# Performance work log

Measured on AMD Instinct MI355X. Metric: run time of the kernel, lower is better.

Reference implementation:

```python
import jax, jax.numpy as jnp
import numpy as np

SEQ_LEN = 2048
WIN = 2
LAYERS = 3
D_MODEL = 512
TDA_DIM = 7
TDA_WEIGHT = 0.3


def _nan0(x):
    return jnp.where(jnp.isnan(x), jnp.zeros_like(x), x)


def _tda_features(x):
    # x: [B, T, D] -> [B, 7]; vectorized version of the per-(b,d) stats loop
    B, T, D = x.shape
    mean = x.mean(axis=1)                                  # [B, D]
    std = x.std(axis=1, ddof=1)                            # torch.std is unbiased
    mn = x.min(axis=1)
    mx = x.max(axis=1)
    idx = jnp.arange(T, dtype=x.dtype)
    xc = x - mean[:, None, :]
    ic = idx - idx.mean()
    trend = _nan0(jnp.einsum('btd,t->bd', xc, ic) /
                  jnp.sqrt((xc * xc).sum(axis=1) * (ic * ic).sum()))
    # lag-1 autocorrelation via corrcoef of (x[:-1], x[1:])
    a = x[:, :-1, :]; b = x[:, 1:, :]
    ac = a - a.mean(axis=1, keepdims=True)
    bc = b - b.mean(axis=1, keepdims=True)
    autocorr = _nan0((ac * bc).sum(axis=1) /
                     jnp.sqrt((ac * ac).sum(axis=1) * (bc * bc).sum(axis=1)))
    # spectral centroid over first T//2 bins of |fft|^2 (== |rfft|^2 there)
    half = T // 2
    ps = jnp.abs(jnp.fft.rfft(x, axis=1)[:, :half, :]) ** 2  # [B, half, D]
    centroid = _nan0(jnp.einsum('btd,t->bd', ps, idx[:half]) / ps.sum(axis=1))
    feats = jnp.stack([mean, std, mn, mx, trend, autocorr, centroid], axis=-1)  # [B, D, 7]
    return feats.mean(axis=1)  # mean over channels -> [B, 7]


def _freq_interp(x, src_len, tgt_len):
    # x: [B, D, src_len] -> [B, D, tgt_len]; zero-pad/truncate in rfft domain
    xf = jnp.fft.rfft(x, axis=2)
    tgt_f = tgt_len // 2 + 1
    copy = min(xf.shape[2], tgt_f)
    out_f = jnp.zeros(x.shape[:2] + (tgt_f,), dtype=xf.dtype).at[:, :, :copy].set(xf[:, :, :copy])
    return jnp.fft.irfft(out_f, n=tgt_len, axis=2) * (src_len / tgt_len)


def _forward(levels, w1, b1, w2, b2, inj_w, inj_b):
    tda = _tda_features(levels[0])                              # [B, 7]
    h = jnp.maximum(tda @ w1 + b1, 0.0)
    attn = jax.nn.sigmoid(h @ w2 + b2)[:, None, :]              # [B, 1, D]
    rev = levels[::-1]
    n = len(rev)
    out_low, out_high = rev[0], rev[1]
    outs = [out_low]
    num_inj = LAYERS + 1
    for i in range(n - 1):
        src = SEQ_LEN // WIN ** (LAYERS - i)
        tgt = SEQ_LEN // WIN ** (LAYERS - i - 1)
        res = _freq_interp(out_low.transpose(0, 2, 1), src, tgt).transpose(0, 2, 1)
        left = (out_high - res) * attn
        safe_idx = (n - i - 2) % num_inj
        left = left + TDA_WEIGHT * (tda @ inj_w[safe_idx] + inj_b[safe_idx])[:, None, :]
        out_low = out_high
        if i + 2 <= n - 1:
            out_high = rev[i + 2]
        outs.append(left)
    return tuple(outs[::-1])


def setup_inputs() -> dict:
    key = jax.random.key(0)
    ks = jax.random.split(key, 20)
    B = 32
    inp = {}
    for l in range(LAYERS + 1):
        T = SEQ_LEN // WIN ** l
        inp[f'level{l}'] = jax.random.normal(ks[l], (B, T, D_MODEL), dtype=jnp.float32)
    s7 = 1.0 / np.sqrt(TDA_DIM)
    sd = 1.0 / np.sqrt(D_MODEL)
    inp['w1'] = jax.random.normal(ks[4], (TDA_DIM, D_MODEL), dtype=jnp.float32) * s7
    inp['b1'] = jnp.zeros((D_MODEL,), dtype=jnp.float32)
    inp['w2'] = jax.random.normal(ks[5], (D_MODEL, D_MODEL), dtype=jnp.float32) * sd
    inp['b2'] = jnp.zeros((D_MODEL,), dtype=jnp.float32)
    for j in range(LAYERS + 1):
        inp[f'wi{j}'] = jax.random.normal(ks[6 + j], (TDA_DIM, D_MODEL), dtype=jnp.float32) * s7
        inp[f'bi{j}'] = jnp.zeros((D_MODEL,), dtype=jnp.float32)
    return inp


def reference(level0, level1, level2, level3, w1, b1, w2, b2,
              wi0, bi0, wi1, bi1, wi2, bi2, wi3, bi3):
    levels = [level0, level1, level2, level3]
    inj_w = [wi0, wi1, wi2, wi3]
    inj_b = [bi0, bi1, bi2, bi3]
    return _forward(levels, w1, b1, w2, b2, inj_w, inj_b)
```

## Files before the change

kernel.cpp:

```cpp
#include <hip/hip_runtime.h>
#include <math.h>

constexpr int B  = 32;
constexpr int T0 = 2048;
constexpr int D  = 512;

constexpr size_t OFF_PART = 0;
constexpr size_t OFF_ATTN = OFF_PART + (size_t)B * 64 * 8;
constexpr size_t OFF_INJ  = OFF_ATTN + (size_t)B * D;

typedef float nfloat4 __attribute__((ext_vector_type(4)));

template<int LO>
__device__ __forceinline__ void wredt_add(float& v) {
  #pragma unroll
  for (int off = 32; off >= LO; off >>= 1) v += __shfl_down(v, off);
}
template<int LO>
__device__ __forceinline__ void wredt_min(float& v) {
  #pragma unroll
  for (int off = 32; off >= LO; off >>= 1) v = fminf(v, __shfl_down(v, off));
}
template<int LO>
__device__ __forceinline__ void wredt_max(float& v) {
  #pragma unroll
  for (int off = 32; off >= LO; off >>= 1) v = fmaxf(v, __shfl_down(v, off));
}
__device__ __forceinline__ void wred_add(float& v) { wredt_add<4>(v); }

__device__ __forceinline__ void nt_store4(float* p, float4 v) {
  nfloat4 nv;
  nv.x = v.x; nv.y = v.y; nv.z = v.z; nv.w = v.w;
  __builtin_nontemporal_store(nv, (nfloat4*)p);
}

__device__ __forceinline__ float4 cadd(float4 a, float4 b) {
  return make_float4(a.x+b.x, a.y+b.y, a.z+b.z, a.w+b.w);
}
__device__ __forceinline__ float4 csub(float4 a, float4 b) {
  return make_float4(a.x-b.x, a.y-b.y, a.z-b.z, a.w-b.w);
}
__device__ __forceinline__ float4 cmul(float4 v, float2 w) {
  return make_float4(v.x*w.x - v.y*w.y, v.x*w.y + v.y*w.x,
                     v.z*w.x - v.w*w.y, v.z*w.y + v.w*w.x);
}
__device__ __forceinline__ float4 cmulc(float4 v, float2 w) {
  return make_float4(v.x*w.x + v.y*w.y, v.y*w.x - v.x*w.y,
                     v.z*w.x + v.w*w.y, v.w*w.x - v.z*w.y);
}
__device__ __forceinline__ float4 cmul_mi(float4 v) {
  return make_float4(v.y, -v.x, v.w, -v.z);
}
__device__ __forceinline__ float4 cmul_pi(float4 v) {
  return make_float4(-v.y, v.x, -v.w, v.z);
}

__global__ __launch_bounds__(512) void k_tda(const float* __restrict__ x,
                                              float* __restrict__ part) {
  __shared__ float4 buf[T0 * 2];
  __shared__ float2 tw[1024];
  __shared__ float perd[8][8];
  float* scr = (float*)tw;
  const int tid  = threadIdx.x;
  const int L = blockIdx.x + 64 * blockIdx.y;
  const int m = (L >> 3) & 1;
  const int q = (L & 7) | ((L >> 4) << 3);
  const int eb = (q & 31) * 2 + m;
  const int b  = q >> 5;
  const int f    = tid & 1;
  const int rIdx = tid >> 1;
  const int lane = tid & 63;
  const int wv   = tid >> 6;
  const float* base = x + (size_t)b * T0 * D + eb * 8 + f * 4;

  float4 s1 = {0,0,0,0}, s2 = {0,0,0,0}, st = {0,0,0,0};
  float4 mn = {INFINITY,INFINITY,INFINITY,INFINITY};
  float4 mx = {-INFINITY,-INFINITY,-INFINITY,-INFINITY};
  #pragma unroll
  for (int u = 0; u < 8; ++u) {
    int t = rIdx + 256 * u;
    float4 v = *(const float4*)&base[(size_t)t * D];
    buf[t * 2 + f] = v;
    float tf = (float)t;
    s1.x += v.x; s1.y += v.y; s1.z += v.z; s1.w += v.w;
    s2.x = fmaf(v.x,v.x,s2.x); s2.y = fmaf(v.y,v.y,s2.y);
    s2.z = fmaf(v.z,v.z,s2.z); s2.w = fmaf(v.w,v.w,s2.w);
    st.x = fmaf(tf,v.x,st.x); st.y = fmaf(tf,v.y,st.y);
    st.z = fmaf(tf,v.z,st.z); st.w = fmaf(tf,v.w,st.w);
    mn.x = fminf(mn.x,v.x); mn.y = fminf(mn.y,v.y); mn.z = fminf(mn.z,v.z); mn.w = fminf(mn.w,v.w);
    mx.x = fmaxf(mx.x,v.x); mx.y = fmaxf(mx.y,v.y); mx.z = fmaxf(mx.z,v.z); mx.w = fmaxf(mx.w,v.w);
  }
  __syncthreads();
  float4 cc = {0,0,0,0};
  #pragma unroll
  for (int u = 0; u < 8; ++u) {
    int t = rIdx + 256 * u;
    if (t < T0 - 1) {
      float4 a = buf[t * 2 + f];
      float4 nb = buf[(t + 1) * 2 + f];
      cc.x = fmaf(a.x,nb.x,cc.x); cc.y = fmaf(a.y,nb.y,cc.y);
      cc.z = fmaf(a.z,nb.z,cc.z); cc.w = fmaf(a.w,nb.w,cc.w);
    }
  }
  wredt_add<2>(s1.x); wredt_add<2>(s1.y); wredt_add<2>(s1.z); wredt_add<2>(s1.w);
  wredt_add<2>(s2.x); wredt_add<2>(s2.y); wredt_add<2>(s2.z); wredt_add<2>(s2.w);
  wredt_add<2>(st.x); wredt_add<2>(st.y); wredt_add<2>(st.z); wredt_add<2>(st.w);
  wredt_add<2>(cc.x); wredt_add<2>(cc.y); wredt_add<2>(cc.z); wredt_add<2>(cc.w);
  wredt_min<2>(mn.x); wredt_min<2>(mn.y); wredt_min<2>(mn.z); wredt_min<2>(mn.w);
  wredt_max<2>(mx.x); wredt_max<2>(mx.y); wredt_max<2>(mx.z); wredt_max<2>(mx.w);
  if (lane < 2) {
    float* p = scr + ((size_t)wv * 2 + f) * 24;
    p[0]=s1.x; p[1]=s2.x; p[2]=st.x; p[3]=cc.x; p[4]=mn.x; p[5]=mx.x;
    p[6]=s1.y; p[7]=s2.y; p[8]=st.y; p[9]=cc.y; p[10]=mn.y; p[11]=mx.y;
    p[12]=s1.z; p[13]=s2.z; p[14]=st.z; p[15]=cc.z; p[16]=mn.z; p[17]=mx.z;
    p[18]=s1.w; p[19]=s2.w; p[20]=st.w; p[21]=cc.w; p[22]=mn.w; p[23]=mx.w;
  }
  __syncthreads();
  if (tid < 8) {
    const int dl = tid;
    const int fq = dl >> 2, c = dl & 3;
    float S1=0.f, S2=0.f, St=0.f, C=0.f, MN=INFINITY, MX=-INFINITY;
    for (int w = 0; w < 8; ++w) {
      const float* p = scr + ((size_t)w * 2 + fq) * 24 + c * 6;
      S1 += p[0]; S2 += p[1]; St += p[2]; C += p[3];
      MN = fminf(MN, p[4]); MX = fmaxf(MX, p[5]);
    }
    const float x0 = ((const float*)buf)[dl];
    const float xl = ((const float*)buf)[(size_t)(T0 - 1) * 8 + dl];
    const float Tf = (float)T0;
    const float mean = S1 / Tf;
    const float sxx  = S2 - S1 * S1 / Tf;
    const float stdv = sqrtf(fmaxf(sxx / (Tf - 1.f), 0.f));
    const float tbar = (Tf - 1.f) * 0.5f;
    const float Sic  = Tf * (Tf * Tf - 1.f) / 12.f;
    float trend = (St - tbar * S1) / sqrtf(sxx * Sic);
    if (isnan(trend)) trend = 0.f;
    const float na = Tf - 1.f;
    const float Sa = S1 - xl, Sb = S1 - x0;
    const float an  = C - Sa * Sb / na;
    const float sa2 = (S2 - xl * xl) - Sa * Sa / na;
    const float sb2 = (S2 - x0 * x0) - Sb * Sb / na;
    float ac = an / sqrtf(sa2 * sb2);
    if (isnan(ac)) ac = 0.f;
    perd[dl][0] = mean; perd[dl][1] = stdv; perd[dl][2] = MN;
    perd[dl][3] = MX;   perd[dl][4] = trend; perd[dl][5] = ac;
  }
  __syncthreads();

  for (int k = tid; k < 1024; k += 512) {
    float sw, cw;
    sincosf(-(float)M_PI * (float)k * (1.0f / 1024.0f), &sw, &cw);
    tw[k] = make_float2(cw, sw);
  }
  __syncthreads();

  for (int stg = 0; stg < 10; stg += 2) {
    const int lg = 10 - stg;
    const int h = 1 << lg;
    #pragma unroll
    for (int it = 0; it < 2; ++it) {
      int sl = it * 512 + tid;
      int pp = sl & 1;
      int qi = sl >> 1;
      int j2 = qi & (h / 2 - 1);
      int g2 = qi >> (lg - 1);
      int bs = (g2 << (lg + 1)) + j2;
      float2 w1 = tw[j2 << stg];
      float2 w2 = tw[j2 << (stg + 1)];
      float4 x0 = buf[bs * 2 + pp];
      float4 x1 = buf[(bs + h/2) * 2 + pp];
      float4 x2 = buf[(bs + h) * 2 + pp];
      float4 x3 = buf[(bs + h + h/2) * 2 + pp];
      float4 u0 = cadd(x0, x2);
      float4 t2 = cmul(csub(x0, x2), w1);
      float4 u1 = cadd(x1, x3);
      float4 t3 = cmul_mi(cmul(csub(x1, x3), w1));
      buf[bs * 2 + pp]             = cadd(u0, u1);
      buf[(bs + h/2) * 2 + pp]     = cmul(csub(u0, u1), w2);
      buf[(bs + h) * 2 + pp]       = cadd(t2, t3);
      buf[(bs + h + h/2) * 2 + pp] = cmul(csub(t2, t3), w2);
    }
    __syncthreads();
  }
  #pragma unroll
  for (int it = 0; it < 4; ++it) {
    int sl = it * 512 + tid;
    int pp = sl & 1;
    int bi = sl >> 1;
    int i = bi * 2;
    float4 a = buf[i * 2 + pp];
    float4 c = buf[(i + 1) * 2 + pp];
    buf[i * 2 + pp]       = cadd(a, c);
    buf[(i + 1) * 2 + pp] = csub(a, c);
  }
  __syncthreads();

  float4 num = {0,0,0,0}, den = {0,0,0,0};
  #pragma unroll
  for (int it = 0; it < 4; ++it) {
    int sl = it * 512 + tid;
    int pp = sl & 1;
    int k = sl >> 1;
    int p1 = __brev((unsigned)k) >> 21;
    int p2 = __brev((unsigned)((T0 - k) & (T0 - 1))) >> 21;
    float4 zk = buf[p1 * 2 + pp];
    float4 zm = buf[p2 * 2 + pp];
    float kf = (float)k;
    float arx = 0.5f*(zk.x+zm.x), ary = 0.5f*(zk.y-zm.y);
    float brx = 0.5f*(zk.y+zm.y), bry = 0.5f*(zm.x-zk.x);
    float pa = arx*arx + ary*ary, pb = brx*brx + bry*bry;
    num.x = fmaf(kf, pa, num.x); den.x += pa;
    num.y = fmaf(kf, pb, num.y); den.y += pb;
    arx = 0.5f*(zk.z+zm.z); ary = 0.5f*(zk.w-zm.w);
    brx = 0.5f*(zk.w+zm.w); bry = 0.5f*(zm.z-zk.z);
    pa = arx*arx + ary*ary; pb = brx*brx + bry*bry;
    num.z = fmaf(kf, pa, num.z); den.z += pa;
    num.w = fmaf(kf, pb, num.w); den.w += pb;
  }
  wredt_add<2>(num.x); wredt_add<2>(num.y); wredt_add<2>(num.z); wredt_add<2>(num.w);
  wredt_add<2>(den.x); wredt_add<2>(den.y); wredt_add<2>(den.z); wredt_add<2>(den.w);
  if (lane < 2) {
    float* p = scr + ((size_t)wv * 2 + f) * 8;
    p[0]=num.x; p[1]=num.y; p[2]=num.z; p[3]=num.w;
    p[4]=den.x; p[5]=den.y; p[6]=den.z; p[7]=den.w;
  }
  __syncthreads();
  if (tid < 8) {
    const int dl = tid;
    const int fq = dl >> 2, c = dl & 3;
    float N = 0.f, Dn = 0.f;
    for (int w = 0; w < 8; ++w) {
      const float* p = scr + ((size_t)w * 2 + fq) * 8;
      N += p[c]; Dn += p[4 + c];
    }
    float cent = N / Dn;
    if (isnan(cent)) cent = 0.f;
    perd[dl][6] = cent;
  }
  __syncthreads();
  if (tid < 7) {
    float s = 0.f;
    #pragma unroll
    for (int dl = 0; dl < 8; ++dl) s += perd[dl][tid];
    part[((size_t)b * 64 + eb) * 8 + tid] = s;
  }
}

__global__ __launch_bounds__(512) void k_weights(const float* __restrict__ part,
    const float* __restrict__ w1, const float* __restrict__ b1,
    const float* __restrict__ w2, const float* __restrict__ b2,
    const float* __restrict__ wi0, const float* __restrict__ bi0,
    const float* __restrict__ wi1, const float* __restrict__ bi1,
    const float* __restrict__ wi2, const float* __restrict__ bi2,
    float* __restrict__ attn, float* __restrict__ inj) {
  const int b = blockIdx.x;
  const int j = threadIdx.x;
  __shared__ float td[7];
  __shared__ float h[512];
  if (j < 7) {
    float s = 0.f;
    for (int w = 0; w < 64; ++w) s += part[((size_t)b * 64 + w) * 8 + j];
    td[j] = s * (1.0f / (float)D);
  }
  __syncthreads();
  float a = b1[j];
  #pragma unroll
  for (int f = 0; f < 7; ++f) a = fmaf(td[f], w1[f * D + j], a);
  h[j] = fmaxf(a, 0.0f);
  __syncthreads();
  float a2 = b2[j];
  for (int k = 0; k < D; ++k) a2 = fmaf(h[k], w2[k * D + j], a2);
  attn[(size_t)b * D + j] = 1.0f / (1.0f + expf(-a2));
  const float* wis[3] = {wi0, wi1, wi2};
  const float* bis[3] = {bi0, bi1, bi2};
  #pragma unroll
  for (int l = 0; l < 3; ++l) {
    float ai = bis[l][j];
    #pragma unroll
    for (int f = 0; f < 7; ++f) ai = fmaf(td[f], wis[l][f * D + j], ai);
    inj[(size_t)l * B * D + (size_t)b * D + j] = 0.3f * ai;
  }
}

template<int S, int NT, bool COPY>
__global__ __launch_bounds__(NT) void k_interp(const float* __restrict__ low,
                                                const float* __restrict__ high,
                                                const float* __restrict__ attn,
                                                const float* __restrict__ inj,
                                                float* __restrict__ out,
                                                float* __restrict__ copy_out) {
  constexpr int LOG2S = (S == 1024) ? 10 : (S == 512) ? 9 : 8;
  constexpr int WAVES = NT / 64;
  constexpr int RPT   = S / (NT / 4);
  __shared__ float4 buf[S * 4];
  __shared__ float2 tw[S];
  __shared__ float4 scrA[WAVES][4];
  __shared__ float4 Zh4[4];
  const int tid  = threadIdx.x;
  const int L = blockIdx.x + 32 * blockIdx.y;
  const int m = (L >> 3) & 1;
  const int q = (L & 7) | ((L >> 4) << 3);
  const int eb = (q & 15) * 2 + m;
  const int b  = q >> 4;
  const int f    = tid & 3;
  const int rIdx = tid >> 2;
  const int lane = tid & 63;
  const int wv   = tid >> 6;
  const int d0   = eb * 16;

  const float* lowb  = low  + (size_t)b * S * D + d0 + 4 * f;
  const float* highb = high + (size_t)b * (2 * S) * D + d0 + 4 * f;
  float*       outb  = out  + (size_t)b * (2 * S) * D + d0 + 4 * f;
  float*       cpb   = COPY ? copy_out + (size_t)b * S * D + d0 + 4 * f : nullptr;

  float4 zreg[RPT];
  float4 acc = {0,0,0,0};
  #pragma unroll
  for (int u = 0; u < RPT; ++u) {
    int t = rIdx + (NT / 4) * u;
    float4 v = *(const float4*)&lowb[(size_t)t * D];
    zreg[u] = v;
    buf[t * 4 + f] = v;
    if (COPY) nt_store4(&cpb[(size_t)t * D], v);
    acc.x += v.x; acc.y += v.y; acc.z += v.z; acc.w += v.w;
  }
  if (rIdx & 1) { acc.x = -acc.x; acc.y = -acc.y; acc.z = -acc.z; acc.w = -acc.w; }
  for (int k = tid; k < S; k += NT) {
    float sw, cw;
    sincosf(-(float)M_PI * (float)k * (1.0f / (float)S), &sw, &cw);
    tw[k] = make_float2(cw, sw);
  }
  wred_add(acc.x); wred_add(acc.y); wred_add(acc.z); wred_add(acc.w);
  if (lane < 4) scrA[wv][f] = acc;
  __syncthreads();
  if (tid < 4) {
    float4 s = scrA[0][tid];
    for (int w = 1; w < WAVES; ++w) {
      float4 qv = scrA[w][tid];
      s.x += qv.x; s.y += qv.y; s.z += qv.z; s.w += qv.w;
    }
    Zh4[tid] = s;
  }
  __syncthreads();

  const float inv4S = 1.0f / (4.0f * (float)S);
  const float4 at4 = *(const float4*)&attn[(size_t)b * D + d0 + 4 * f];
  const float4 in4 = *(const float4*)&inj [(size_t)b * D + d0 + 4 * f];
  float4 Zs = Zh4[f];
  Zs.x *= inv4S; Zs.y *= inv4S; Zs.z *= inv4S; Zs.w *= inv4S;

  for (int stg = 0; stg + 1 < LOG2S; stg += 2) {
    const int lg = LOG2S - 1 - stg;
    const int h = 1 << lg;
    #pragma unroll
    for (int it = 0; it < S / NT; ++it) {
      int sl = it * NT + tid;
      int pp = sl & 3;
      int qi = sl >> 2;
      int j2 = qi & (h / 2 - 1);
      int g2 = qi >> (lg - 1);
      int bs = (g2 << (lg + 1)) + j2;
      float2 w1 = tw[j2 << (stg + 1)];
      float2 w2 = tw[j2 << (stg + 2)];
      float4 x0 = buf[bs * 4 + pp];
      float4 x1 = buf[(bs + h/2) * 4 + pp];
      float4 x2 = buf[(bs + h) * 4 + pp];
      float4 x3 = buf[(bs + h + h/2) * 4 + pp];
      float4 u0 = cadd(x0, x2);
      float4 t2 = cmul(csub(x0, x2), w1);
      float4 u1 = cadd(x1, x3);
      float4 t3 = cmul_mi(cmul(csub(x1, x3), w1));
      buf[bs * 4 + pp]             = cadd(u0, u1);
      buf[(bs + h/2) * 4 + pp]     = cmul(csub(u0, u1), w2);
      buf[(bs + h) * 4 + pp]       = cadd(t2, t3);
      buf[(bs + h + h/2) * 4 + pp] = cmul(csub(t2, t3), w2);
    }
    __syncthreads();
  }
  if (LOG2S & 1) {
    #pragma unroll
    for (int it = 0; it < (2 * S) / NT; ++it) {
      int sl = it * NT + tid;
      int pp = sl & 3;
      int bi = sl >> 2;
      int i = bi * 2;
      float4 a = buf[i * 4 + pp];
      float4 c4 = buf[(i + 1) * 4 + pp];
      buf[i * 4 + pp]       = cadd(a, c4);
      buf[(i + 1) * 4 + pp] = csub(a, c4);
    }
    __syncthreads();
  }

  {
    #pragma unroll
    for (int it = 0; it < S / NT; ++it) {
      int sl = it * NT + tid;
      int pp = sl & 3;
      int qi = sl >> 2;
      int bs = qi * 4;
      float4 x[4];
      #pragma unroll
      for (int e = 0; e < 4; ++e) {
        int p = bs + e;
        int k = __brev((unsigned)p) >> (32 - LOG2S);
        float2 w = tw[k];
        float sgn = (k < S / 2) ? 1.f : (k == S / 2) ? 0.f : -1.f;
        float4 v = cmulc(buf[p * 4 + pp], w);
        v.x *= sgn; v.y *= sgn; v.z *= sgn; v.w *= sgn;
        x[e] = v;
      }
      float4 u0 = cadd(x[0], x[1]), u1 = csub(x[0], x[1]);
      float4 u2 = cadd(x[2], x[3]), u3 = csub(x[2], x[3]);
      float4 s3 = cmul_pi(u3);
      buf[(bs + 0) * 4 + pp] = cadd(u0, u2);
      buf[(bs + 1) * 4 + pp] = cadd(u1, s3);
      buf[(bs + 2) * 4 + pp] = csub(u0, u2);
      buf[(bs + 3) * 4 + pp] = csub(u1, s3);
    }
    __syncthreads();
  }

  for (int stg = 2; stg + 1 < LOG2S; stg += 2) {
    const int h = 1 << stg;
    #pragma unroll
    for (int it = 0; it < S / NT; ++it) {
      int sl = it * NT + tid;
      int pp = sl & 3;
      int qi = sl >> 2;
      int j = qi & (h - 1);
      int g = qi >> stg;
      int bs = (g << (stg + 2)) + j;
      float2 wA = tw[j << (LOG2S - stg)];
      float2 wB = tw[j << (LOG2S - stg - 1)];
      float4 x0 = buf[bs * 4 + pp];
      float4 x1 = buf[(bs + h) * 4 + pp];
      float4 x2 = buf[(bs + 2 * h) * 4 + pp];
      float4 x3 = buf[(bs + 3 * h) * 4 + pp];
      float4 t1 = cmulc(x1, wA);
      float4 u0 = cadd(x0, t1), u1 = csub(x0, t1);
      float4 t3 = cmulc(x3, wA);
      float4 u2 = cadd(x2, t3), u3 = csub(x2, t3);
      float4 s2 = cmulc(u2, wB);
      float4 s3 = cmul_pi(cmulc(u3, wB));
      buf[bs * 4 + pp]           = cadd(u0, s2);
      buf[(bs + h) * 4 + pp]     = cadd(u1, s3);
      buf[(bs + 2 * h) * 4 + pp] = csub(u0, s2);
      buf[(bs + 3 * h) * 4 + pp] = csub(u1, s3);
    }
    __syncthreads();
  }
  if (LOG2S & 1) {
    const int stg = LOG2S - 1;
    const int h = 1 << stg;
    #pragma unroll
    for (int it = 0; it < (2 * S) / NT; ++it) {
      int sl = it * NT + tid;
      int pp = sl & 3;
      int bi = sl >> 2;
      int j = bi & (h - 1);
      int g = bi >> stg;
      int i = (g << (stg + 1)) + j;
      float2 w = tw[j << (LOG2S - stg)];
      float4 a = buf[i * 4 + pp];
      float4 v = buf[(i + h) * 4 + pp];
      float4 t = cmulc(v, w);
      buf[i * 4 + pp]       = cadd(a, t);
      buf[(i + h) * 4 + pp] = csub(a, t);
    }
    __syncthreads();
  }

  #pragma unroll
  for (int u = 0; u < RPT; ++u) {
    int j = rIdx + (NT / 4) * u;
    float4 z = zreg[u];
    float sg = (j & 1) ? -1.f : 1.f;
    float4 res_e;
    res_e.x = fmaf(0.25f, z.x, sg * Zs.x);
    res_e.y = fmaf(0.25f, z.y, sg * Zs.y);
    res_e.z = fmaf(0.25f, z.z, sg * Zs.z);
    res_e.w = fmaf(0.25f, z.w, sg * Zs.w);
    float4 y = buf[j * 4 + f];
    float4 h0 = *(const float4*)&highb[(size_t)(2 * j) * D];
    float4 h1 = *(const float4*)&highb[(size_t)(2 * j + 1) * D];
    float4 o0, o1;
    o0.x = fmaf(h0.x - res_e.x, at4.x, in4.x);
    o0.y = fmaf(h0.y - res_e.y, at4.y, in4.y);
    o0.z = fmaf(h0.z - res_e.z, at4.z, in4.z);
    o0.w = fmaf(h0.w - res_e.w, at4.w, in4.w);
    o1.x = fmaf(h1.x - y.x * inv4S, at4.x, in4.x);
    o1.y = fmaf(h1.y - y.y * inv4S, at4.y, in4.y);
    o1.z = fmaf(h1.z - y.z * inv4S, at4.z, in4.z);
    o1.w = fmaf(h1.w - y.w * inv4S, at4.w, in4.w);
    nt_store4(&outb[(size_t)(2 * j) * D], o0);
    nt_store4(&outb[(size_t)(2 * j + 1) * D], o1);
  }
}

extern "C" void kernel_launch(void* const* d_in, const int* in_sizes, int n_in,
                              void* d_out, int out_size, void* d_ws, size_t ws_size,
                              hipStream_t stream) {
  const float* level0 = (const float*)d_in[0];
  const float* level1 = (const float*)d_in[1];
  const float* level2 = (const float*)d_in[2];
  const float* level3 = (const float*)d_in[3];
  const float* w1  = (const float*)d_in[4];
  const float* b1  = (const float*)d_in[5];
  const float* w2  = (const float*)d_in[6];
  const float* b2  = (const float*)d_in[7];
  const float* wi0 = (const float*)d_in[8];
  const float* bi0 = (const float*)d_in[9];
  const float* wi1 = (const float*)d_in[10];
  const float* bi1 = (const float*)d_in[11];
  const float* wi2 = (const float*)d_in[12];
  const float* bi2 = (const float*)d_in[13];

  float* ws   = (float*)d_ws;
  float* part = ws + OFF_PART;
  float* attn = ws + OFF_ATTN;
  float* inj  = ws + OFF_INJ;

  float* out0 = (float*)d_out;
  float* out1 = out0 + (size_t)B * 2048 * D;
  float* out2 = out1 + (size_t)B * 1024 * D;
  float* out3 = out2 + (size_t)B * 512 * D;

  k_tda<<<dim3(64, B), 512, 0, stream>>>(level0, part);
  k_weights<<<B, 512, 0, stream>>>(part, w1, b1, w2, b2, wi0, bi0, wi1, bi1, wi2, bi2,
                                   attn, inj);

  k_interp<1024, 512, false><<<dim3(32, B), 512, 0, stream>>>(
      level1, level0, attn, inj + 0ull * B * D, out0, nullptr);
  k_interp<512, 512, false><<<dim3(32, B), 512, 0, stream>>>(
      level2, level1, attn, inj + 1ull * B * D, out1, nullptr);
  k_interp<256, 256, true><<<dim3(32, B), 256, 0, stream>>>(
      level3, level2, attn, inj + 2ull * B * D, out2, out3);
}
```

Before: 259.5 us.

## Replace radix-4 FFT passes with radix-8 passes in shared memory

Both the TDA spectral kernel and the interpolation kernels now run their forward and inverse FFT stages as radix-8 butterflies held in registers instead of radix-4. A 2-point or 4-point cleanup stage covers the leftover log2 sizes. This cuts the number of shared-memory read/write passes and block barriers per transform. In exchange, each thread holds eight float4 values at once, which raises register pressure. In the interpolation kernel some threads also sit idle when S/2 is not a multiple of the block size.

```diff
diff --git a/kernel.cpp b/kernel.cpp
--- a/kernel.cpp
+++ b/kernel.cpp
@@ -53,6 +53,42 @@
 }
 __device__ __forceinline__ float4 cmul_pi(float4 v) {
   return make_float4(-v.y, v.x, -v.w, v.z);
+}
+
+#define R8C 0.70710678118654752f
+
+__device__ __forceinline__ void r8_fwd(float4 x[8], float2 tA, float2 tB, float2 tC) {
+  float4 a0 = cadd(x[0], x[4]), a1 = cadd(x[1], x[5]);
+  float4 a2 = cadd(x[2], x[6]), a3 = cadd(x[3], x[7]);
+  float4 b0 = cmul(csub(x[0], x[4]), tA);
+  float4 b1 = cmul(cmul(csub(x[1], x[5]), tA), make_float2(R8C, -R8C));
+  float4 b2 = cmul_mi(cmul(csub(x[2], x[6]), tA));
+  float4 b3 = cmul(cmul(csub(x[3], x[7]), tA), make_float2(-R8C, -R8C));
+  float4 p0 = cadd(a0, a2), p1 = cmul(csub(a0, a2), tB);
+  float4 p2 = cadd(a1, a3), p3 = cmul_mi(cmul(csub(a1, a3), tB));
+  x[0] = cadd(p0, p2); x[1] = cmul(csub(p0, p2), tC);
+  x[2] = cadd(p1, p3); x[3] = cmul(csub(p1, p3), tC);
+  float4 q0 = cadd(b0, b2), q1 = cmul(csub(b0, b2), tB);
+  float4 q2 = cadd(b1, b3), q3 = cmul_mi(cmul(csub(b1, b3), tB));
+  x[4] = cadd(q0, q2); x[5] = cmul(csub(q0, q2), tC);
+  x[6] = cadd(q1, q3); x[7] = cmul(csub(q1, q3), tC);
+}
+
+__device__ __forceinline__ void r8_inv(float4 x[8], float2 wA, float2 wB, float2 wC) {
+  float4 t1 = cmulc(x[1], wA); float4 u0 = cadd(x[0], t1), u1 = csub(x[0], t1);
+  float4 t3 = cmulc(x[3], wA); float4 u2 = cadd(x[2], t3), u3 = csub(x[2], t3);
+  float4 t5 = cmulc(x[5], wA); float4 u4 = cadd(x[4], t5), u5 = csub(x[4], t5);
+  float4 t7 = cmulc(x[7], wA); float4 u6 = cadd(x[6], t7), u7 = csub(x[6], t7);
+  float4 s2 = cmulc(u2, wB), s3 = cmul_pi(cmulc(u3, wB));
+  float4 y0 = cadd(u0, s2), y1 = cadd(u1, s3), y2 = csub(u0, s2), y3 = csub(u1, s3);
+  float4 s6 = cmulc(u6, wB), s7 = cmul_pi(cmulc(u7, wB));
+  float4 y4 = cadd(u4, s6), y5 = cadd(u5, s7), y6 = csub(u4, s6), y7 = csub(u5, s7);
+  float4 c0 = cmulc(y4, wC);
+  float4 c1 = cmul(cmulc(y5, wC), make_float2(R8C, R8C));
+  float4 c2 = cmul_pi(cmulc(y6, wC));
+  float4 c3 = cmul(cmulc(y7, wC), make_float2(-R8C, R8C));
+  x[0] = cadd(y0, c0); x[1] = cadd(y1, c1); x[2] = cadd(y2, c2); x[3] = cadd(y3, c3);
+  x[4] = csub(y0, c0); x[5] = csub(y1, c1); x[6] = csub(y2, c2); x[7] = csub(y3, c3);
 }
 
 __global__ __launch_bounds__(512) void k_tda(const float* __restrict__ x,
@@ -154,44 +190,41 @@
   }
   __syncthreads();
 
-  for (int stg = 0; stg < 10; stg += 2) {
-    const int lg = 10 - stg;
-    const int h = 1 << lg;
-    #pragma unroll
-    for (int it = 0; it < 2; ++it) {
-      int sl = it * 512 + tid;
-      int pp = sl & 1;
-      int qi = sl >> 1;
-      int j2 = qi & (h / 2 - 1);
-      int g2 = qi >> (lg - 1);
-      int bs = (g2 << (lg + 1)) + j2;
-      float2 w1 = tw[j2 << stg];
-      float2 w2 = tw[j2 << (stg + 1)];
-      float4 x0 = buf[bs * 2 + pp];
-      float4 x1 = buf[(bs + h/2) * 2 + pp];
-      float4 x2 = buf[(bs + h) * 2 + pp];
-      float4 x3 = buf[(bs + h + h/2) * 2 + pp];
-      float4 u0 = cadd(x0, x2);
-      float4 t2 = cmul(csub(x0, x2), w1);
-      float4 u1 = cadd(x1, x3);
-      float4 t3 = cmul_mi(cmul(csub(x1, x3), w1));
-      buf[bs * 2 + pp]             = cadd(u0, u1);
-      buf[(bs + h/2) * 2 + pp]     = cmul(csub(u0, u1), w2);
-      buf[(bs + h) * 2 + pp]       = cadd(t2, t3);
-      buf[(bs + h + h/2) * 2 + pp] = cmul(csub(t2, t3), w2);
-    }
+  for (int stg = 0; stg < 9; stg += 3) {
+    const int qsh = 8 - stg;
+    const int Q = 1 << qsh;
+    int pp = tid & 1;
+    int gi = tid >> 1;
+    int j3 = gi & (Q - 1);
+    int g  = gi >> qsh;
+    int bs = (g << (qsh + 3)) + j3;
+    float2 tA = tw[j3 << stg];
+    float2 tB = tw[j3 << (stg + 1)];
+    float2 tC = tw[j3 << (stg + 2)];
+    float4 xx[8];
+    #pragma unroll
+    for (int mm = 0; mm < 8; ++mm) xx[mm] = buf[(bs + mm * Q) * 2 + pp];
+    r8_fwd(xx, tA, tB, tC);
+    #pragma unroll
+    for (int mm = 0; mm < 8; ++mm) buf[(bs + mm * Q) * 2 + pp] = xx[mm];
     __syncthreads();
   }
   #pragma unroll
-  for (int it = 0; it < 4; ++it) {
+  for (int it = 0; it < 2; ++it) {
     int sl = it * 512 + tid;
     int pp = sl & 1;
-    int bi = sl >> 1;
-    int i = bi * 2;
-    float4 a = buf[i * 2 + pp];
-    float4 c = buf[(i + 1) * 2 + pp];
-    buf[i * 2 + pp]       = cadd(a, c);
-    buf[(i + 1) * 2 + pp] = csub(a, c);
+    int qi = sl >> 1;
+    int bs = qi << 2;
+    float4 x0 = buf[bs*2+pp], x1 = buf[(bs+1)*2+pp];
+    float4 x2 = buf[(bs+2)*2+pp], x3 = buf[(bs+3)*2+pp];
+    float4 u0 = cadd(x0, x2);
+    float4 t2 = csub(x0, x2);
+    float4 u1 = cadd(x1, x3);
+    float4 t3 = cmul_mi(csub(x1, x3));
+    buf[bs*2+pp]     = cadd(u0, u1);
+    buf[(bs+1)*2+pp] = csub(u0, u1);
+    buf[(bs+2)*2+pp] = cadd(t2, t3);
+    buf[(bs+3)*2+pp] = csub(t2, t3);
   }
   __syncthreads();
 
@@ -292,6 +325,7 @@
   constexpr int LOG2S = (S == 1024) ? 10 : (S == 512) ? 9 : 8;
   constexpr int WAVES = NT / 64;
   constexpr int RPT   = S / (NT / 4);
+  constexpr int R8IT  = S / 2;
   __shared__ float4 buf[S * 4];
   __shared__ float2 tw[S];
   __shared__ float4 scrA[WAVES][4];
@@ -349,35 +383,32 @@
   float4 Zs = Zh4[f];
   Zs.x *= inv4S; Zs.y *= inv4S; Zs.z *= inv4S; Zs.w *= inv4S;
 
-  for (int stg = 0; stg + 1 < LOG2S; stg += 2) {
-    const int lg = LOG2S - 1 - stg;
-    const int h = 1 << lg;
-    #pragma unroll
-    for (int it = 0; it < S / NT; ++it) {
+  for (int stg = 0; stg + 2 < LOG2S; stg += 3) {
+    const int qsh = LOG2S - 3 - stg;
+    const int Q = 1 << qsh;
+    #pragma unroll
+    for (int it = 0; it < (R8IT + NT - 1) / NT; ++it) {
       int sl = it * NT + tid;
-      int pp = sl & 3;
-      int qi = sl >> 2;
-      int j2 = qi & (h / 2 - 1);
-      int g2 = qi >> (lg - 1);
-      int bs = (g2 << (lg + 1)) + j2;
-      float2 w1 = tw[j2 << (stg + 1)];
-      float2 w2 = tw[j2 << (stg + 2)];
-      float4 x0 = buf[bs * 4 + pp];
-      float4 x1 = buf[(bs + h/2) * 4 + pp];
-      float4 x2 = buf[(bs + h) * 4 + pp];
-      float4 x3 = buf[(bs + h + h/2) * 4 + pp];
-      float4 u0 = cadd(x0, x2);
-      float4 t2 = cmul(csub(x0, x2), w1);
-      float4 u1 = cadd(x1, x3);
-      float4 t3 = cmul_mi(cmul(csub(x1, x3), w1));
-      buf[bs * 4 + pp]             = cadd(u0, u1);
-      buf[(bs + h/2) * 4 + pp]     = cmul(csub(u0, u1), w2);
-      buf[(bs + h) * 4 + pp]       = cadd(t2, t3);
-      buf[(bs + h + h/2) * 4 + pp] = cmul(csub(t2, t3), w2);
-    }
-    __syncthreads();
-  }
-  if (LOG2S & 1) {
+      if (sl < R8IT) {
+        int pp = sl & 3;
+        int gi = sl >> 2;
+        int j3 = gi & (Q - 1);
+        int g  = gi >> qsh;
+        int bs = (g << (qsh + 3)) + j3;
+        float2 tA = tw[j3 << (stg + 1)];
+        float2 tB = tw[j3 << (stg + 2)];
+        float2 tC = tw[j3 << (stg + 3)];
+        float4 xx[8];
+        #pragma unroll
+        for (int mm = 0; mm < 8; ++mm) xx[mm] = buf[(bs + mm * Q) * 4 + pp];
+        r8_fwd(xx, tA, tB, tC);
+        #pragma unroll
+        for (int mm = 0; mm < 8; ++mm) buf[(bs + mm * Q) * 4 + pp] = xx[mm];
+      }
+      __syncthreads();
+    }
+  }
+  if (LOG2S % 3 == 1) {
     #pragma unroll
     for (int it = 0; it < (2 * S) / NT; ++it) {
       int sl = it * NT + tid;
@@ -391,37 +422,86 @@
     }
     __syncthreads();
   }
-
-  {
+  if (LOG2S % 3 == 2) {
     #pragma unroll
     for (int it = 0; it < S / NT; ++it) {
       int sl = it * NT + tid;
       int pp = sl & 3;
       int qi = sl >> 2;
-      int bs = qi * 4;
-      float4 x[4];
-      #pragma unroll
-      for (int e = 0; e < 4; ++e) {
-        int p = bs + e;
-        int k = __brev((unsigned)p) >> (32 - LOG2S);
-        float2 w = tw[k];
-        float sgn = (k < S / 2) ? 1.f : (k == S / 2) ? 0.f : -1.f;
-        float4 v = cmulc(buf[p * 4 + pp], w);
-        v.x *= sgn; v.y *= sgn; v.z *= sgn; v.w *= sgn;
-        x[e] = v;
+      int bs = qi << 2;
+      float4 x0 = buf[bs*4+pp], x1 = buf[(bs+1)*4+pp];
+      float4 x2 = buf[(bs+2)*4+pp], x3 = buf[(bs+3)*4+pp];
+      float4 u0 = cadd(x0, x2);
+      float4 t2 = csub(x0, x2);
+      float4 u1 = cadd(x1, x3);
+      float4 t3 = cmul_mi(csub(x1, x3));
+      buf[bs*4+pp]     = cadd(u0, u1);
+      buf[(bs+1)*4+pp] = csub(u0, u1);
+      buf[(bs+2)*4+pp] = cadd(t2, t3);
+      buf[(bs+3)*4+pp] = csub(t2, t3);
+    }
+    __syncthreads();
+  }
+
+  for (int stg = 0; stg + 2 < LOG2S; stg += 3) {
+    const int h = 1 << stg;
+    #pragma unroll
+    for (int it = 0; it < (R8IT + NT - 1) / NT; ++it) {
+      int sl = it * NT + tid;
+      if (sl < R8IT) {
+        int pp = sl & 3;
+        int gi = sl >> 2;
+        int j  = gi & (h - 1);
+        int G  = gi >> stg;
+        int bs = (G << (stg + 3)) + j;
+        float2 wA = tw[j << (LOG2S - stg)];
+        float2 wB = tw[j << (LOG2S - stg - 1)];
+        float2 wC = tw[j << (LOG2S - stg - 2)];
+        float4 xx[8];
+        if (stg == 0) {
+          #pragma unroll
+          for (int mm = 0; mm < 8; ++mm) {
+            int p = bs + mm;
+            int k = __brev((unsigned)p) >> (32 - LOG2S);
+            float2 w = tw[k];
+            float sgn = (k < S / 2) ? 1.f : (k == S / 2) ? 0.f : -1.f;
+            float4 v = cmulc(buf[p * 4 + pp], w);
+            v.x *= sgn; v.y *= sgn; v.z *= sgn; v.w *= sgn;
+            xx[mm] = v;
+          }
+        } else {
+          #pragma unroll
+          for (int mm = 0; mm < 8; ++mm) xx[mm] = buf[(bs + mm * h) * 4 + pp];
+        }
+        r8_inv(xx, wA, wB, wC);
+        #pragma unroll
+        for (int mm = 0; mm < 8; ++mm) buf[(bs + mm * h) * 4 + pp] = xx[mm];
       }
-      float4 u0 = cadd(x[0], x[1]), u1 = csub(x[0], x[1]);
-      float4 u2 = cadd(x[2], x[3]), u3 = csub(x[2], x[3]);
-      float4 s3 = cmul_pi(u3);
-      buf[(bs + 0) * 4 + pp] = cadd(u0, u2);
-      buf[(bs + 1) * 4 + pp] = cadd(u1, s3);
-      buf[(bs + 2) * 4 + pp] = csub(u0, u2);
-      buf[(bs + 3) * 4 + pp] = csub(u1, s3);
+      __syncthreads();
+    }
+  }
+  if (LOG2S % 3 == 1) {
+    const int stg = LOG2S - 1;
+    const int h = 1 << stg;
+    #pragma unroll
+    for (int it = 0; it < (2 * S) / NT; ++it) {
+      int sl = it * NT + tid;
+      int pp = sl & 3;
+      int bi = sl >> 2;
+      int j = bi & (h - 1);
+      int g = bi >> stg;
+      int i = (g << (stg + 1)) + j;
+      float2 w = tw[j << (LOG2S - stg)];
+      float4 a = buf[i * 4 + pp];
+      float4 v = buf[(i + h) * 4 + pp];
+      float4 t = cmulc(v, w);
+      buf[i * 4 + pp]       = cadd(a, t);
+      buf[(i + h) * 4 + pp] = csub(a, t);
     }
     __syncthreads();
   }
-
-  for (int stg = 2; stg + 1 < LOG2S; stg += 2) {
+  if (LOG2S % 3 == 2) {
+    const int stg = LOG2S - 2;
     const int h = 1 << stg;
     #pragma unroll
     for (int it = 0; it < S / NT; ++it) {
@@ -441,32 +521,12 @@
       float4 u0 = cadd(x0, t1), u1 = csub(x0, t1);
       float4 t3 = cmulc(x3, wA);
       float4 u2 = cadd(x2, t3), u3 = csub(x2, t3);
-      float4 s2 = cmulc(u2, wB);
-      float4 s3 = cmul_pi(cmulc(u3, wB));
-      buf[bs * 4 + pp]           = cadd(u0, s2);
-      buf[(bs + h) * 4 + pp]     = cadd(u1, s3);
-      buf[(bs + 2 * h) * 4 + pp] = csub(u0, s2);
-      buf[(bs + 3 * h) * 4 + pp] = csub(u1, s3);
-    }
-    __syncthreads();
-  }
-  if (LOG2S & 1) {
-    const int stg = LOG2S - 1;
-    const int h = 1 << stg;
-    #pragma unroll
-    for (int it = 0; it < (2 * S) / NT; ++it) {
-      int sl = it * NT + tid;
-      int pp = sl & 3;
-      int bi = sl >> 2;
-      int j = bi & (h - 1);
-      int g = bi >> stg;
-      int i = (g << (stg + 1)) + j;
-      float2 w = tw[j << (LOG2S - stg)];
-      float4 a = buf[i * 4 + pp];
-      float4 v = buf[(i + h) * 4 + pp];
-      float4 t = cmulc(v, w);
-      buf[i * 4 + pp]       = cadd(a, t);
-      buf[(i + h) * 4 + pp] = csub(a, t);
+      float4 s2c = cmulc(u2, wB);
+      float4 s3c = cmul_pi(cmulc(u3, wB));
+      buf[bs * 4 + pp]           = cadd(u0, s2c);
+      buf[(bs + h) * 4 + pp]     = cadd(u1, s3c);
+      buf[(bs + 2 * h) * 4 + pp] = csub(u0, s2c);
+      buf[(bs + 3 * h) * 4 + pp] = csub(u1, s3c);
     }
     __syncthreads();
   }
```

Measured after the change: 257.8 us, median of 2. Within noise of the previous version (-0.7%).
